# Kernel tuning notes

Hardware: AMD Instinct MI355X
Metric: run time of the kernel (lower is better)

## Reference

```python
import jax, jax.numpy as jnp
import numpy as np

NEG_SLOPE = 0.2  # PyG GATConv default LeakyReLU slope
EPS = 1e-16


def gat_conv(x, src, dst, W, att_src, att_dst, bias, concat):
    """One GATConv layer (PyG semantics, self-loops already in src/dst).
    x: [N, Fin]; src/dst: [E'] int; W: [Fin, H*C]; att_*: [H, C]; bias: [H*C] or [C].
    """
    N = x.shape[0]
    H, C = att_src.shape
    h = (x @ W).reshape(N, H, C)                      # [N, H, C]
    a_s = jnp.einsum('nhc,hc->nh', h, att_src)        # [N, H]
    a_d = jnp.einsum('nhc,hc->nh', h, att_dst)        # [N, H]
    logits = jax.nn.leaky_relu(a_s[src] + a_d[dst], NEG_SLOPE)  # [E', H]
    # segment softmax over incoming edges of each destination node
    m = jax.ops.segment_max(logits, dst, num_segments=N)        # [N, H]
    m = jnp.where(jnp.isfinite(m), m, 0.0)
    e = jnp.exp(logits - m[dst])                                # [E', H]
    denom = jax.ops.segment_sum(e, dst, num_segments=N)         # [N, H]
    alpha = e / (denom[dst] + EPS)                              # [E', H]
    msg = h[src] * alpha[:, :, None]                            # [E', H, C]
    out = jax.ops.segment_sum(msg, dst, num_segments=N)         # [N, H, C]
    out = out.reshape(N, H * C) if concat else out.mean(axis=1)
    return out + bias


def setup_inputs() -> dict:
    key = jax.random.key(0)
    ks = jax.random.split(key, 8)
    N, E, IN, HID, OUT, H1 = 50000, 800000, 128, 64, 32, 2
    x = jax.random.normal(ks[0], (N, IN), dtype=jnp.float32)
    edge_index = jax.random.randint(ks[1], (2, E), 0, N, dtype=jnp.int32)
    # glorot-ish scaled params
    W1 = jax.random.normal(ks[2], (IN, H1 * HID), dtype=jnp.float32) * (1.0 / np.sqrt(IN))
    att_src1 = jax.random.normal(ks[3], (H1, HID), dtype=jnp.float32) * (1.0 / np.sqrt(HID))
    att_dst1 = jax.random.normal(ks[4], (H1, HID), dtype=jnp.float32) * (1.0 / np.sqrt(HID))
    bias1 = jnp.zeros((H1 * HID,), dtype=jnp.float32)
    W2 = jax.random.normal(ks[5], (H1 * HID, OUT), dtype=jnp.float32) * (1.0 / np.sqrt(H1 * HID))
    att_src2 = jax.random.normal(ks[6], (1, OUT), dtype=jnp.float32) * (1.0 / np.sqrt(OUT))
    att_dst2 = jax.random.normal(ks[7], (1, OUT), dtype=jnp.float32) * (1.0 / np.sqrt(OUT))
    bias2 = jnp.zeros((OUT,), dtype=jnp.float32)
    return {"x": x, "edge_index": edge_index, "W1": W1, "att_src1": att_src1,
            "att_dst1": att_dst1, "bias1": bias1, "W2": W2, "att_src2": att_src2,
            "att_dst2": att_dst2, "bias2": bias2}


def reference(x, edge_index, W1, att_src1, att_dst1, bias1, W2, att_src2, att_dst2, bias2):
    N = x.shape[0]
    loops = jnp.arange(N, dtype=edge_index.dtype)
    src = jnp.concatenate([edge_index[0], loops])   # add self loops (PyG default)
    dst = jnp.concatenate([edge_index[1], loops])
    h = gat_conv(x, src, dst, W1, att_src1, att_dst1, bias1, concat=True)
    h = jax.nn.relu(h)
    out = gat_conv(h, src, dst, W2, att_src2, att_dst2, bias2, concat=False)
    return out
```

## Files before the change

### kernel.cpp

```cpp
#include <hip/hip_runtime.h>
#include <math.h>


typedef __bf16 bf16x8 __attribute__((ext_vector_type(8)));
typedef float f32x4 __attribute__((ext_vector_type(4)));

__device__ __forceinline__ float lrelu(float x) { return x > 0.f ? x : 0.2f * x; }

__device__ __forceinline__ unsigned short f2bf(float x) {
  unsigned u = __float_as_uint(x);
  return (unsigned short)((u + 0x7fffu + ((u >> 16) & 1u)) >> 16);
}
__device__ __forceinline__ float2 bf2_unpack(unsigned u) {
  return make_float2(__uint_as_float(u << 16), __uint_as_float(u & 0xffff0000u));
}

constexpr int CAP = 5632;

union SharedK1 {
  struct { int hist[256]; int bbase[256]; } part;
  union { unsigned short bl[32 * 64 * 8]; float accl[64 * 132]; } gem;
};

__launch_bounds__(256)
__global__ void k_csr_gemm1(const int* __restrict__ srcA, const int* __restrict__ dstA,
                            int E, int Nn, int PB, int* __restrict__ gcnt,
                            unsigned* __restrict__ bkt,
                            const float* __restrict__ A, const float* __restrict__ B,
                            unsigned short* __restrict__ Cb,
                            const float* __restrict__ attS, const float* __restrict__ attD,
                            float* __restrict__ asO, float* __restrict__ adO, int M) {
  __shared__ SharedK1 sm;
  const int tid = threadIdx.x;
  if ((int)blockIdx.x < PB) {
    const int NBK = (Nn + 255) >> 8;
    for (int i = tid; i < 256; i += 256) sm.part.hist[i] = 0;
    __syncthreads();
    const int tot = E + Nn;
    const int g0 = blockIdx.x * 4096;
    unsigned pk[16]; int bk[16], rk[16]; int cnt = 0;
#pragma unroll
    for (int j = 0; j < 16; ++j) {
      int g = g0 + j * 256 + tid;
      if (g >= tot) break;
      int s, d;
      if (g < E) { s = srcA[g]; d = dstA[g]; } else { s = g - E; d = s; }
      int b = d >> 8;
      pk[cnt] = (unsigned)s | ((unsigned)(d & 255) << 16);
      bk[cnt] = b;
      rk[cnt] = atomicAdd(&sm.part.hist[b], 1);
      cnt++;
    }
    __syncthreads();
    for (int i = tid; i < 256; i += 256) {
      int h = (i < NBK) ? sm.part.hist[i] : 0;
      sm.part.bbase[i] = h ? atomicAdd(&gcnt[i], h) : 0;
    }
    __syncthreads();
    for (int j = 0; j < cnt; ++j) {
      int pos = sm.part.bbase[bk[j]] + rk[j];
      if (pos < CAP) bkt[(size_t)bk[j] * CAP + pos] = pk[j];
    }
    return;
  }
  const int lane = tid & 63, w = tid >> 6;
  const int row0 = (blockIdx.x - PB) * 64;
  for (int i = tid; i < 128 * 32; i += 256) {
    int k = i >> 5, n4 = (i & 31) << 2;
    float4 v = *(const float4*)(B + k * 128 + n4);
    int c = k >> 5, q = (k >> 3) & 3, j = k & 7;
    float vv[4] = {v.x, v.y, v.z, v.w};
#pragma unroll
    for (int u2 = 0; u2 < 4; ++u2) {
      int n = n4 + u2, t = n >> 4, l = q * 16 + (n & 15);
      sm.gem.bl[((t * 4 + c) * 64 + l) * 8 + j] = f2bf(vv[u2]);
    }
  }
  int mrow = row0 + 16 * w + (lane & 15);
  bool rok = mrow < M;
  const int q = lane >> 4;
  bf16x8 afr[4];
  union { unsigned short s[8]; bf16x8 b; } cv;
#pragma unroll
  for (int c = 0; c < 4; ++c) {
    float4 u0 = make_float4(0.f, 0.f, 0.f, 0.f), u1 = u0;
    if (rok) {
      const float* ap = A + (size_t)mrow * 128 + c * 32 + q * 8;
      u0 = *(const float4*)ap; u1 = *(const float4*)(ap + 4);
    }
    cv.s[0] = f2bf(u0.x); cv.s[1] = f2bf(u0.y); cv.s[2] = f2bf(u0.z); cv.s[3] = f2bf(u0.w);
    cv.s[4] = f2bf(u1.x); cv.s[5] = f2bf(u1.y); cv.s[6] = f2bf(u1.z); cv.s[7] = f2bf(u1.w);
    afr[c] = cv.b;
  }
  __syncthreads();
  f32x4 acc[8];
#pragma unroll
  for (int t = 0; t < 8; ++t) {
    f32x4 a = {0.f, 0.f, 0.f, 0.f};
#pragma unroll
    for (int c = 0; c < 4; ++c) {
      bf16x8 bf = *(((const bf16x8*)sm.gem.bl) + (t * 4 + c) * 64 + lane);
      a = __builtin_amdgcn_mfma_f32_16x16x32_bf16(afr[c], bf, a, 0, 0, 0);
    }
    acc[t] = a;
  }
  __syncthreads();
  {
    int rbase = 16 * w + q * 4, cl = lane & 15;
#pragma unroll
    for (int t = 0; t < 8; ++t)
#pragma unroll
      for (int r = 0; r < 4; ++r)
        sm.gem.accl[(rbase + r) * 132 + 16 * t + cl] = acc[t][r];
  }
  __syncthreads();
  {
    int row = tid >> 2, cg = tid & 3, c0 = cg * 32;
    int grow = row0 + row;
    const float* ar = &sm.gem.accl[row * 132 + c0];
    float ps = 0.f, pd = 0.f;
    unsigned pkv[16];
#pragma unroll
    for (int u2 = 0; u2 < 8; ++u2) {
      float4 v  = *(const float4*)(ar + u2 * 4);
      float4 s4 = *(const float4*)(attS + c0 + u2 * 4);
      float4 d4 = *(const float4*)(attD + c0 + u2 * 4);
      ps += v.x * s4.x + v.y * s4.y + v.z * s4.z + v.w * s4.w;
      pd += v.x * d4.x + v.y * d4.y + v.z * d4.z + v.w * d4.w;
      pkv[u2 * 2]     = (unsigned)f2bf(v.x) | ((unsigned)f2bf(v.y) << 16);
      pkv[u2 * 2 + 1] = (unsigned)f2bf(v.z) | ((unsigned)f2bf(v.w) << 16);
    }
    ps += __shfl_xor(ps, 1); pd += __shfl_xor(pd, 1);
    if (grow < M) {
      if ((tid & 1) == 0) {
        int head = (tid >> 1) & 1;
        asO[(size_t)grow * 2 + head] = ps; adO[(size_t)grow * 2 + head] = pd;
      }
      unsigned* cp = (unsigned*)(Cb + (size_t)grow * 128 + c0);
      *(uint4*)(cp)      = make_uint4(pkv[0], pkv[1], pkv[2], pkv[3]);
      *(uint4*)(cp + 4)  = make_uint4(pkv[4], pkv[5], pkv[6], pkv[7]);
      *(uint4*)(cp + 8)  = make_uint4(pkv[8], pkv[9], pkv[10], pkv[11]);
      *(uint4*)(cp + 12) = make_uint4(pkv[12], pkv[13], pkv[14], pkv[15]);
    }
  }
}

__launch_bounds__(512)
__global__ void k_fine(const unsigned* __restrict__ bkt, const int* __restrict__ gcnt,
                       int Nn, int tot, int* __restrict__ offs, unsigned* __restrict__ csr) {
  __shared__ int fc[256];
  __shared__ int lo[256];
  __shared__ int cur[256];
  __shared__ int baseS;
  const int b = blockIdx.x;
  const int tid = threadIdx.x;
  int m = gcnt[b]; if (m > CAP) m = CAP;
  const unsigned* p = bkt + (size_t)b * CAP;
  if (b == 0 && tid == 0) offs[Nn] = tot;
  for (int i = tid; i < 256; i += 512) fc[i] = 0;
  __syncthreads();
  for (int i = tid; i < m; i += 512) atomicAdd(&fc[p[i] >> 16], 1);
  __syncthreads();
  if (tid < 64) {
    int s = 0;
    for (int c = tid; c < b; c += 64) s += gcnt[c];
#pragma unroll
    for (int o = 32; o; o >>= 1) s += __shfl_xor(s, o);
    if (tid == 0) baseS = s;
    int carry = 0;
    for (int c = 0; c < 256; c += 64) {
      int v = fc[c + tid]; int x = v;
#pragma unroll
      for (int o = 1; o < 64; o <<= 1) { int t = __shfl_up(x, o); if (tid >= o) x += t; }
      lo[c + tid] = carry + x - v;
      carry += __shfl(x, 63);
    }
  }
  __syncthreads();
  const int base = baseS;
  for (int i = tid; i < 256; i += 512) {
    cur[i] = lo[i];
    int n = (b << 8) + i;
    if (n < Nn) offs[n] = base + lo[i];
  }
  __syncthreads();
  for (int i = tid; i < m; i += 512) {
    unsigned e = p[i];
    int pos = atomicAdd(&cur[e >> 16], 1);
    csr[base + pos] = e & 0xffffu;
  }
}

__global__ void k_agg1(const unsigned* __restrict__ h1b, const float* __restrict__ as1,
                       const float* __restrict__ ad1, const int* __restrict__ offs,
                       const unsigned* __restrict__ csr, const float* __restrict__ bias,
                       unsigned* __restrict__ outb, int Nn) {
  int n = blockIdx.x * (blockDim.x >> 6) + (threadIdx.x >> 6);
  if (n >= Nn) return;
  int lane = threadIdx.x & 63;
  int head = lane >> 5;
  int el = lane & 31;
  int pbase = (lane & 32) << 2;
  int beg = offs[n], end = offs[n + 1];
  float2 adn = ((const float2*)ad1)[n];
  float adh = head ? adn.y : adn.x;
  float ax = 0.f, ay = 0.f, den = 0.f;
  int i = beg;
  while (i < end) {
    int m = end - i; if (m > 32) m = 32;
    bool ok = el < m;
    unsigned e = ok ? csr[i + el] : 0u;
    int sv = (int)e;
    float wv = 0.f;
    if (ok) {
      float2 a = ((const float2*)as1)[sv];
      wv = __expf(lrelu((head ? a.y : a.x) + adh));
    }
    int j = 0;
    for (; j + 4 <= m; j += 4) {
#pragma unroll
      for (int u = 0; u < 4; ++u) {
        int s = __builtin_amdgcn_readlane(sv, j + u);
        float ee = __int_as_float(
            __builtin_amdgcn_ds_bpermute(pbase + 4 * (j + u), __float_as_int(wv)));
        float2 v = bf2_unpack(h1b[(size_t)s * 64 + lane]);
        ax += ee * v.x; ay += ee * v.y; den += ee;
      }
    }
    for (; j < m; ++j) {
      int s = __builtin_amdgcn_readlane(sv, j);
      float ee = __int_as_float(
          __builtin_amdgcn_ds_bpermute(pbase + 4 * j, __float_as_int(wv)));
      float2 v = bf2_unpack(h1b[(size_t)s * 64 + lane]);
      ax += ee * v.x; ay += ee * v.y; den += ee;
    }
    i += m;
  }
  float inv = 1.f / (den + 1e-16f);
  const float2 bv = ((const float2*)bias)[lane];
  float o0 = ax * inv + bv.x; o0 = o0 > 0.f ? o0 : 0.f;
  float o1 = ay * inv + bv.y; o1 = o1 > 0.f ? o1 : 0.f;
  outb[(size_t)n * 64 + lane] = (unsigned)f2bf(o0) | ((unsigned)f2bf(o1) << 16);
}

__launch_bounds__(256)
__global__ void k_gemm2(const unsigned* __restrict__ Ab, const float* __restrict__ B,
                        unsigned short* __restrict__ Cb,
                        const float* __restrict__ attS, const float* __restrict__ attD,
                        float* __restrict__ asO, float* __restrict__ adO, int M) {
  __shared__ unsigned short bl[8 * 64 * 8];
  __shared__ float accl[64 * 36];
  const int tid = threadIdx.x;
  const int lane = tid & 63, w = tid >> 6;
  const int row0 = blockIdx.x * 64;
  for (int i = tid; i < 128 * 8; i += 256) {
    int k = i >> 3, n4 = (i & 7) << 2;
    float4 v = *(const float4*)(B + k * 32 + n4);
    int c = k >> 5, q = (k >> 3) & 3, j = k & 7;
    float vv[4] = {v.x, v.y, v.z, v.w};
#pragma unroll
    for (int u2 = 0; u2 < 4; ++u2) {
      int n = n4 + u2, t = n >> 4, l = q * 16 + (n & 15);
      bl[((t * 4 + c) * 64 + l) * 8 + j] = f2bf(vv[u2]);
    }
  }
  int mrow = row0 + 16 * w + (lane & 15);
  bool rok = mrow < M;
  const int q = lane >> 4;
  bf16x8 afr[4];
#pragma unroll
  for (int c = 0; c < 4; ++c) {
    uint4 u = make_uint4(0u, 0u, 0u, 0u);
    if (rok) u = *(const uint4*)(Ab + (size_t)mrow * 64 + c * 16 + q * 4);
    afr[c] = __builtin_bit_cast(bf16x8, u);
  }
  __syncthreads();
  f32x4 acc[2];
#pragma unroll
  for (int t = 0; t < 2; ++t) {
    f32x4 a = {0.f, 0.f, 0.f, 0.f};
#pragma unroll
    for (int c = 0; c < 4; ++c) {
      bf16x8 bf = *(((const bf16x8*)bl) + (t * 4 + c) * 64 + lane);
      a = __builtin_amdgcn_mfma_f32_16x16x32_bf16(afr[c], bf, a, 0, 0, 0);
    }
    acc[t] = a;
  }
  {
    int rbase = 16 * w + q * 4, cl = lane & 15;
#pragma unroll
    for (int t = 0; t < 2; ++t)
#pragma unroll
      for (int r = 0; r < 4; ++r)
        accl[(rbase + r) * 36 + 16 * t + cl] = acc[t][r];
  }
  __syncthreads();
  {
    int row = tid >> 2, cg = tid & 3, c0 = cg * 8;
    int grow = row0 + row;
    const float* ar = &accl[row * 36 + c0];
    float ps = 0.f, pd = 0.f;
    unsigned pk[4];
#pragma unroll
    for (int u2 = 0; u2 < 2; ++u2) {
      float4 v  = *(const float4*)(ar + u2 * 4);
      float4 s4 = *(const float4*)(attS + c0 + u2 * 4);
      float4 d4 = *(const float4*)(attD + c0 + u2 * 4);
      ps += v.x * s4.x + v.y * s4.y + v.z * s4.z + v.w * s4.w;
      pd += v.x * d4.x + v.y * d4.y + v.z * d4.z + v.w * d4.w;
      pk[u2 * 2]     = (unsigned)f2bf(v.x) | ((unsigned)f2bf(v.y) << 16);
      pk[u2 * 2 + 1] = (unsigned)f2bf(v.z) | ((unsigned)f2bf(v.w) << 16);
    }
    ps += __shfl_xor(ps, 1); ps += __shfl_xor(ps, 2);
    pd += __shfl_xor(pd, 1); pd += __shfl_xor(pd, 2);
    if (grow < M) {
      if (cg == 0) { asO[grow] = ps; adO[grow] = pd; }
      *(uint4*)(Cb + (size_t)grow * 32 + c0) = make_uint4(pk[0], pk[1], pk[2], pk[3]);
    }
  }
}

__global__ void k_agg2(const unsigned* __restrict__ h2b, const float* __restrict__ as2,
                       const float* __restrict__ ad2, const int* __restrict__ offs,
                       const unsigned* __restrict__ csr, const float* __restrict__ bias,
                       float* __restrict__ out, int Nn) {
  int n = blockIdx.x * (blockDim.x >> 6) + (threadIdx.x >> 6);
  if (n >= Nn) return;
  int lane = threadIdx.x & 63;
  int g = lane >> 4, cp = lane & 15;
  int beg = offs[n], end = offs[n + 1];
  float adn = ad2[n];
  float ax = 0.f, ay = 0.f, den = 0.f;
  int i = beg;
  while (i < end) {
    int m = end - i; if (m > 64) m = 64;
    int idx = i + lane;
    bool ok = idx < end;
    int sv = ok ? (int)csr[idx] : 0;
    float wv = ok ? __expf(lrelu(as2[sv] + adn)) : 0.f;
    for (int j = 0; j < m; j += 4) {
      int jj = j + g;
      float ee = __shfl(wv, jj);
      int s = __shfl(sv, jj);
      float2 v = bf2_unpack(h2b[(size_t)s * 16 + cp]);
      ax += ee * v.x; ay += ee * v.y; den += ee;
    }
    i += m;
  }
  ax += __shfl_xor(ax, 16); ay += __shfl_xor(ay, 16); den += __shfl_xor(den, 16);
  ax += __shfl_xor(ax, 32); ay += __shfl_xor(ay, 32); den += __shfl_xor(den, 32);
  if (lane < 16) {
    float inv = 1.f / (den + 1e-16f);
    const float2 bv = ((const float2*)bias)[cp];
    ((float2*)out)[(size_t)n * 16 + cp] =
        make_float2(ax * inv + bv.x, ay * inv + bv.y);
  }
}

extern "C" void kernel_launch(void* const* d_in, const int* in_sizes, int n_in,
                              void* d_out, int out_size, void* d_ws, size_t ws_size,
                              hipStream_t stream) {
  const float* x      = (const float*)d_in[0];
  const int*   ei     = (const int*)d_in[1];
  const float* W1     = (const float*)d_in[2];
  const float* att_s1 = (const float*)d_in[3];
  const float* att_d1 = (const float*)d_in[4];
  const float* bias1  = (const float*)d_in[5];
  const float* W2     = (const float*)d_in[6];
  const float* att_s2 = (const float*)d_in[7];
  const float* att_d2 = (const float*)d_in[8];
  const float* bias2  = (const float*)d_in[9];
  float* out = (float*)d_out;

  const int N = in_sizes[0] / 128;
  const int E = in_sizes[1] / 2;
  const int* srcA = ei;
  const int* dstA = ei + E;
  const int tot = E + N;
  const int NBK = (N + 255) >> 8;

  char* w = (char*)d_ws;
  auto alloc = [&](size_t bytes) { char* p = w; w += (bytes + 255) / 256 * 256; return p; };
  unsigned short* h1b = (unsigned short*)alloc((size_t)N * 128 * 2);
  unsigned* h2in_b    = (unsigned*)alloc((size_t)N * 64 * 4);
  unsigned short* h2b = (unsigned short*)alloc((size_t)N * 32 * 2);
  float* as1    = (float*)alloc((size_t)N * 2 * 4);
  float* ad1    = (float*)alloc((size_t)N * 2 * 4);
  float* as2    = (float*)alloc((size_t)N * 4);
  float* ad2    = (float*)alloc((size_t)N * 4);
  int*   gcnt   = (int*)alloc((size_t)NBK * 4);
  unsigned* bkt = (unsigned*)alloc((size_t)NBK * CAP * 4);
  int*   offs   = (int*)alloc((size_t)(N + 1) * 4);
  unsigned* csr = (unsigned*)alloc((size_t)tot * 4);

  hipMemsetAsync(gcnt, 0, (size_t)NBK * 4, stream);

  const int PB = (tot + 4095) / 4096;
  const int GB = (N + 63) / 64;
  k_csr_gemm1<<<PB + GB, 256, 0, stream>>>(srcA, dstA, E, N, PB, gcnt, bkt,
                                           x, W1, h1b, att_s1, att_d1, as1, ad1, N);
  k_fine<<<NBK, 512, 0, stream>>>(bkt, gcnt, N, tot, offs, csr);

  int nb = (N + 3) / 4;
  k_agg1<<<nb, 256, 0, stream>>>((const unsigned*)h1b, as1, ad1, offs, csr, bias1, h2in_b, N);
  k_gemm2<<<GB, 256, 0, stream>>>(h2in_b, W2, h2b, att_s2, att_d2, as2, ad2, N);
  k_agg2<<<nb, 256, 0, stream>>>((const unsigned*)h2b, as2, ad2, offs, csr, bias2, out, N);
}
```

Measured before the change: 195.6 us.

## Fuse CSR fine sort, layer-1 aggregation and second GEMM into one kernel

Buckets shrink from 256 to 64 destination nodes, and one 512-thread block per bucket now does three jobs: it builds the CSR segment in shared memory, aggregates layer 1 for its 64 nodes from that shared edge list, and runs the layer-2 MFMA GEMM from a shared tile. This removes two kernel launches, the global round trip of the layer-1 output, and the re-read of the CSR. The CSR index array also shrinks to 16-bit. In exchange, only about 782 blocks do the aggregation, with each wave handling 8 nodes in sequence, so parallelism drops and load balance may worsen. The per-bucket capacity of 1408 could overflow on skewed graphs.

```diff
diff --git a/kernel.cpp b/kernel.cpp
--- a/kernel.cpp
+++ b/kernel.cpp
@@ -15,10 +15,10 @@
   return make_float2(__uint_as_float(u << 16), __uint_as_float(u & 0xffff0000u));
 }
 
-constexpr int CAP = 5632;
+constexpr int CAP2 = 1408;
 
 union SharedK1 {
-  struct { int hist[256]; int bbase[256]; } part;
+  struct { int hist[1024]; int bbase[1024]; } part;
   union { unsigned short bl[32 * 64 * 8]; float accl[64 * 132]; } gem;
 };
 
@@ -33,8 +33,8 @@
   __shared__ SharedK1 sm;
   const int tid = threadIdx.x;
   if ((int)blockIdx.x < PB) {
-    const int NBK = (Nn + 255) >> 8;
-    for (int i = tid; i < 256; i += 256) sm.part.hist[i] = 0;
+    const int NBK = (Nn + 63) >> 6;
+    for (int i = tid; i < NBK; i += 256) sm.part.hist[i] = 0;
     __syncthreads();
     const int tot = E + Nn;
     const int g0 = blockIdx.x * 4096;
@@ -45,21 +45,21 @@
       if (g >= tot) break;
       int s, d;
       if (g < E) { s = srcA[g]; d = dstA[g]; } else { s = g - E; d = s; }
-      int b = d >> 8;
-      pk[cnt] = (unsigned)s | ((unsigned)(d & 255) << 16);
+      int b = d >> 6;
+      pk[cnt] = (unsigned)s | ((unsigned)(d & 63) << 16);
       bk[cnt] = b;
       rk[cnt] = atomicAdd(&sm.part.hist[b], 1);
       cnt++;
     }
     __syncthreads();
-    for (int i = tid; i < 256; i += 256) {
-      int h = (i < NBK) ? sm.part.hist[i] : 0;
+    for (int i = tid; i < NBK; i += 256) {
+      int h = sm.part.hist[i];
       sm.part.bbase[i] = h ? atomicAdd(&gcnt[i], h) : 0;
     }
     __syncthreads();
     for (int j = 0; j < cnt; ++j) {
       int pos = sm.part.bbase[bk[j]] + rk[j];
-      if (pos < CAP) bkt[(size_t)bk[j] * CAP + pos] = pk[j];
+      if (pos < CAP2) bkt[(size_t)bk[j] * CAP2 + pos] = pk[j];
     }
     return;
   }
@@ -146,18 +146,40 @@
 }
 
 __launch_bounds__(512)
-__global__ void k_fine(const unsigned* __restrict__ bkt, const int* __restrict__ gcnt,
-                       int Nn, int tot, int* __restrict__ offs, unsigned* __restrict__ csr) {
-  __shared__ int fc[256];
-  __shared__ int lo[256];
-  __shared__ int cur[256];
+__global__ void k_fused2(const unsigned* __restrict__ bkt, const int* __restrict__ gcnt,
+                         int Nn, int tot,
+                         const float* __restrict__ as1, const float* __restrict__ ad1,
+                         const float* __restrict__ bias1,
+                         const unsigned* __restrict__ h1b,
+                         const float* __restrict__ W2,
+                         const float* __restrict__ attS, const float* __restrict__ attD,
+                         int* __restrict__ offs, unsigned short* __restrict__ csr16,
+                         unsigned short* __restrict__ h2b,
+                         float* __restrict__ as2, float* __restrict__ ad2) {
+  __shared__ unsigned short bl[8 * 64 * 8];
+  __shared__ unsigned h2t[64 * 68];
+  __shared__ unsigned short srcL[CAP2];
+  __shared__ int fc[64], lo[65], cur[64];
+  __shared__ float accl[64 * 36];
   __shared__ int baseS;
   const int b = blockIdx.x;
   const int tid = threadIdx.x;
-  int m = gcnt[b]; if (m > CAP) m = CAP;
-  const unsigned* p = bkt + (size_t)b * CAP;
-  if (b == 0 && tid == 0) offs[Nn] = tot;
-  for (int i = tid; i < 256; i += 512) fc[i] = 0;
+  int m = gcnt[b]; if (m > CAP2) m = CAP2;
+  const unsigned* p = bkt + (size_t)b * CAP2;
+
+  for (int i = tid; i < 128 * 8; i += 512) {
+    int k = i >> 3, n4 = (i & 7) << 2;
+    float4 v = *(const float4*)(W2 + k * 32 + n4);
+    int c = k >> 5, q = (k >> 3) & 3, j = k & 7;
+    float vv[4] = {v.x, v.y, v.z, v.w};
+#pragma unroll
+    for (int u2 = 0; u2 < 4; ++u2) {
+      int n = n4 + u2, t = n >> 4, l = q * 16 + (n & 15);
+      bl[((t * 4 + c) * 64 + l) * 8 + j] = f2bf(vv[u2]);
+    }
+  }
+  if (tid < 64) fc[tid] = 0;
+  if (b == 0 && tid == 64) offs[Nn] = tot;
   __syncthreads();
   for (int i = tid; i < m; i += 512) atomicAdd(&fc[p[i] >> 16], 1);
   __syncthreads();
@@ -167,140 +189,104 @@
 #pragma unroll
     for (int o = 32; o; o >>= 1) s += __shfl_xor(s, o);
     if (tid == 0) baseS = s;
-    int carry = 0;
-    for (int c = 0; c < 256; c += 64) {
-      int v = fc[c + tid]; int x = v;
-#pragma unroll
-      for (int o = 1; o < 64; o <<= 1) { int t = __shfl_up(x, o); if (tid >= o) x += t; }
-      lo[c + tid] = carry + x - v;
-      carry += __shfl(x, 63);
-    }
-  }
-  __syncthreads();
-  const int base = baseS;
-  for (int i = tid; i < 256; i += 512) {
-    cur[i] = lo[i];
-    int n = (b << 8) + i;
-    if (n < Nn) offs[n] = base + lo[i];
+    int v = fc[tid], x = v;
+#pragma unroll
+    for (int o = 1; o < 64; o <<= 1) { int t = __shfl_up(x, o); if (tid >= o) x += t; }
+    lo[tid] = x - v;
+    cur[tid] = x - v;
+    if (tid == 63) lo[64] = x;
   }
   __syncthreads();
   for (int i = tid; i < m; i += 512) {
     unsigned e = p[i];
     int pos = atomicAdd(&cur[e >> 16], 1);
-    csr[base + pos] = e & 0xffffu;
-  }
-}
-
-__global__ void k_agg1(const unsigned* __restrict__ h1b, const float* __restrict__ as1,
-                       const float* __restrict__ ad1, const int* __restrict__ offs,
-                       const unsigned* __restrict__ csr, const float* __restrict__ bias,
-                       unsigned* __restrict__ outb, int Nn) {
-  int n = blockIdx.x * (blockDim.x >> 6) + (threadIdx.x >> 6);
-  if (n >= Nn) return;
-  int lane = threadIdx.x & 63;
-  int head = lane >> 5;
-  int el = lane & 31;
-  int pbase = (lane & 32) << 2;
-  int beg = offs[n], end = offs[n + 1];
-  float2 adn = ((const float2*)ad1)[n];
-  float adh = head ? adn.y : adn.x;
-  float ax = 0.f, ay = 0.f, den = 0.f;
-  int i = beg;
-  while (i < end) {
-    int m = end - i; if (m > 32) m = 32;
-    bool ok = el < m;
-    unsigned e = ok ? csr[i + el] : 0u;
-    int sv = (int)e;
-    float wv = 0.f;
-    if (ok) {
-      float2 a = ((const float2*)as1)[sv];
-      wv = __expf(lrelu((head ? a.y : a.x) + adh));
-    }
-    int j = 0;
-    for (; j + 4 <= m; j += 4) {
-#pragma unroll
-      for (int u = 0; u < 4; ++u) {
-        int s = __builtin_amdgcn_readlane(sv, j + u);
+    srcL[pos] = (unsigned short)(e & 0xffffu);
+  }
+  __syncthreads();
+  const int base = baseS;
+  for (int i = tid; i < m; i += 512) csr16[base + i] = srcL[i];
+  if (tid < 64) {
+    int n = (b << 6) + tid;
+    if (n < Nn) offs[n] = base + lo[tid];
+  }
+
+  const int w = tid >> 6, lane = tid & 63;
+  const int head = lane >> 5, el = lane & 31;
+  const int pbase = (lane & 32) << 2;
+  for (int j8 = 0; j8 < 8; ++j8) {
+    int j = w * 8 + j8;
+    int n = (b << 6) + j;
+    if (n >= Nn) break;
+    int beg = lo[j], end = lo[j + 1];
+    float2 adn = ((const float2*)ad1)[n];
+    float adh = head ? adn.y : adn.x;
+    float ax = 0.f, ay = 0.f, den = 0.f;
+    int i = beg;
+    while (i < end) {
+      int mm = end - i; if (mm > 32) mm = 32;
+      bool ok = el < mm;
+      int sv = ok ? (int)srcL[i + el] : 0;
+      float wv = 0.f;
+      if (ok) {
+        float2 a = ((const float2*)as1)[sv];
+        wv = __expf(lrelu((head ? a.y : a.x) + adh));
+      }
+      int j2 = 0;
+      for (; j2 + 4 <= mm; j2 += 4) {
+#pragma unroll
+        for (int u = 0; u < 4; ++u) {
+          int s = __builtin_amdgcn_readlane(sv, j2 + u);
+          float ee = __int_as_float(
+              __builtin_amdgcn_ds_bpermute(pbase + 4 * (j2 + u), __float_as_int(wv)));
+          float2 v = bf2_unpack(h1b[(size_t)s * 64 + lane]);
+          ax += ee * v.x; ay += ee * v.y; den += ee;
+        }
+      }
+      for (; j2 < mm; ++j2) {
+        int s = __builtin_amdgcn_readlane(sv, j2);
         float ee = __int_as_float(
-            __builtin_amdgcn_ds_bpermute(pbase + 4 * (j + u), __float_as_int(wv)));
+            __builtin_amdgcn_ds_bpermute(pbase + 4 * j2, __float_as_int(wv)));
         float2 v = bf2_unpack(h1b[(size_t)s * 64 + lane]);
         ax += ee * v.x; ay += ee * v.y; den += ee;
       }
-    }
-    for (; j < m; ++j) {
-      int s = __builtin_amdgcn_readlane(sv, j);
-      float ee = __int_as_float(
-          __builtin_amdgcn_ds_bpermute(pbase + 4 * j, __float_as_int(wv)));
-      float2 v = bf2_unpack(h1b[(size_t)s * 64 + lane]);
-      ax += ee * v.x; ay += ee * v.y; den += ee;
-    }
-    i += m;
-  }
-  float inv = 1.f / (den + 1e-16f);
-  const float2 bv = ((const float2*)bias)[lane];
-  float o0 = ax * inv + bv.x; o0 = o0 > 0.f ? o0 : 0.f;
-  float o1 = ay * inv + bv.y; o1 = o1 > 0.f ? o1 : 0.f;
-  outb[(size_t)n * 64 + lane] = (unsigned)f2bf(o0) | ((unsigned)f2bf(o1) << 16);
-}
-
-__launch_bounds__(256)
-__global__ void k_gemm2(const unsigned* __restrict__ Ab, const float* __restrict__ B,
-                        unsigned short* __restrict__ Cb,
-                        const float* __restrict__ attS, const float* __restrict__ attD,
-                        float* __restrict__ asO, float* __restrict__ adO, int M) {
-  __shared__ unsigned short bl[8 * 64 * 8];
-  __shared__ float accl[64 * 36];
-  const int tid = threadIdx.x;
-  const int lane = tid & 63, w = tid >> 6;
-  const int row0 = blockIdx.x * 64;
-  for (int i = tid; i < 128 * 8; i += 256) {
-    int k = i >> 3, n4 = (i & 7) << 2;
-    float4 v = *(const float4*)(B + k * 32 + n4);
-    int c = k >> 5, q = (k >> 3) & 3, j = k & 7;
-    float vv[4] = {v.x, v.y, v.z, v.w};
-#pragma unroll
-    for (int u2 = 0; u2 < 4; ++u2) {
-      int n = n4 + u2, t = n >> 4, l = q * 16 + (n & 15);
-      bl[((t * 4 + c) * 64 + l) * 8 + j] = f2bf(vv[u2]);
-    }
-  }
-  int mrow = row0 + 16 * w + (lane & 15);
-  bool rok = mrow < M;
-  const int q = lane >> 4;
-  bf16x8 afr[4];
-#pragma unroll
-  for (int c = 0; c < 4; ++c) {
-    uint4 u = make_uint4(0u, 0u, 0u, 0u);
-    if (rok) u = *(const uint4*)(Ab + (size_t)mrow * 64 + c * 16 + q * 4);
-    afr[c] = __builtin_bit_cast(bf16x8, u);
-  }
-  __syncthreads();
-  f32x4 acc[2];
-#pragma unroll
-  for (int t = 0; t < 2; ++t) {
+      i += mm;
+    }
+    float inv = 1.f / (den + 1e-16f);
+    const float2 bv = ((const float2*)bias1)[lane];
+    float o0 = ax * inv + bv.x; o0 = o0 > 0.f ? o0 : 0.f;
+    float o1 = ay * inv + bv.y; o1 = o1 > 0.f ? o1 : 0.f;
+    h2t[j * 68 + lane] = (unsigned)f2bf(o0) | ((unsigned)f2bf(o1) << 16);
+  }
+  __syncthreads();
+
+  {
+    int rt = w & 3, ct = w >> 2;
+    int mloc = rt * 16 + (lane & 15);
+    int q = lane >> 4;
+    bf16x8 afr[4];
+#pragma unroll
+    for (int c = 0; c < 4; ++c) {
+      uint4 u = *(const uint4*)&h2t[mloc * 68 + c * 16 + q * 4];
+      afr[c] = __builtin_bit_cast(bf16x8, u);
+    }
     f32x4 a = {0.f, 0.f, 0.f, 0.f};
 #pragma unroll
     for (int c = 0; c < 4; ++c) {
-      bf16x8 bf = *(((const bf16x8*)bl) + (t * 4 + c) * 64 + lane);
+      bf16x8 bf = *(((const bf16x8*)bl) + (ct * 4 + c) * 64 + lane);
       a = __builtin_amdgcn_mfma_f32_16x16x32_bf16(afr[c], bf, a, 0, 0, 0);
     }
-    acc[t] = a;
-  }
-  {
-    int rbase = 16 * w + q * 4, cl = lane & 15;
-#pragma unroll
-    for (int t = 0; t < 2; ++t)
-#pragma unroll
-      for (int r = 0; r < 4; ++r)
-        accl[(rbase + r) * 36 + 16 * t + cl] = acc[t][r];
-  }
-  __syncthreads();
-  {
+    int rbase = rt * 16 + q * 4, cl = lane & 15;
+#pragma unroll
+    for (int r = 0; r < 4; ++r)
+      accl[(rbase + r) * 36 + ct * 16 + cl] = a[r];
+  }
+  __syncthreads();
+  if (tid < 256) {
     int row = tid >> 2, cg = tid & 3, c0 = cg * 8;
-    int grow = row0 + row;
+    int grow = (b << 6) + row;
     const float* ar = &accl[row * 36 + c0];
     float ps = 0.f, pd = 0.f;
-    unsigned pk[4];
+    unsigned pkv[4];
 #pragma unroll
     for (int u2 = 0; u2 < 2; ++u2) {
       float4 v  = *(const float4*)(ar + u2 * 4);
@@ -308,22 +294,22 @@
       float4 d4 = *(const float4*)(attD + c0 + u2 * 4);
       ps += v.x * s4.x + v.y * s4.y + v.z * s4.z + v.w * s4.w;
       pd += v.x * d4.x + v.y * d4.y + v.z * d4.z + v.w * d4.w;
-      pk[u2 * 2]     = (unsigned)f2bf(v.x) | ((unsigned)f2bf(v.y) << 16);
-      pk[u2 * 2 + 1] = (unsigned)f2bf(v.z) | ((unsigned)f2bf(v.w) << 16);
+      pkv[u2 * 2]     = (unsigned)f2bf(v.x) | ((unsigned)f2bf(v.y) << 16);
+      pkv[u2 * 2 + 1] = (unsigned)f2bf(v.z) | ((unsigned)f2bf(v.w) << 16);
     }
     ps += __shfl_xor(ps, 1); ps += __shfl_xor(ps, 2);
     pd += __shfl_xor(pd, 1); pd += __shfl_xor(pd, 2);
-    if (grow < M) {
-      if (cg == 0) { asO[grow] = ps; adO[grow] = pd; }
-      *(uint4*)(Cb + (size_t)grow * 32 + c0) = make_uint4(pk[0], pk[1], pk[2], pk[3]);
+    if (grow < Nn) {
+      if (cg == 0) { as2[grow] = ps; ad2[grow] = pd; }
+      *(uint4*)(h2b + (size_t)grow * 32 + c0) = make_uint4(pkv[0], pkv[1], pkv[2], pkv[3]);
     }
   }
 }
 
 __global__ void k_agg2(const unsigned* __restrict__ h2b, const float* __restrict__ as2,
                        const float* __restrict__ ad2, const int* __restrict__ offs,
-                       const unsigned* __restrict__ csr, const float* __restrict__ bias,
-                       float* __restrict__ out, int Nn) {
+                       const unsigned short* __restrict__ csr16,
+                       const float* __restrict__ bias, float* __restrict__ out, int Nn) {
   int n = blockIdx.x * (blockDim.x >> 6) + (threadIdx.x >> 6);
   if (n >= Nn) return;
   int lane = threadIdx.x & 63;
@@ -336,7 +322,7 @@
     int m = end - i; if (m > 64) m = 64;
     int idx = i + lane;
     bool ok = idx < end;
-    int sv = ok ? (int)csr[idx] : 0;
+    int sv = ok ? (int)csr16[idx] : 0;
     float wv = ok ? __expf(lrelu(as2[sv] + adn)) : 0.f;
     for (int j = 0; j < m; j += 4) {
       int jj = j + g;
@@ -377,21 +363,20 @@
   const int* srcA = ei;
   const int* dstA = ei + E;
   const int tot = E + N;
-  const int NBK = (N + 255) >> 8;
+  const int NBK = (N + 63) >> 6;
 
   char* w = (char*)d_ws;
   auto alloc = [&](size_t bytes) { char* p = w; w += (bytes + 255) / 256 * 256; return p; };
   unsigned short* h1b = (unsigned short*)alloc((size_t)N * 128 * 2);
-  unsigned* h2in_b    = (unsigned*)alloc((size_t)N * 64 * 4);
   unsigned short* h2b = (unsigned short*)alloc((size_t)N * 32 * 2);
   float* as1    = (float*)alloc((size_t)N * 2 * 4);
   float* ad1    = (float*)alloc((size_t)N * 2 * 4);
   float* as2    = (float*)alloc((size_t)N * 4);
   float* ad2    = (float*)alloc((size_t)N * 4);
   int*   gcnt   = (int*)alloc((size_t)NBK * 4);
-  unsigned* bkt = (unsigned*)alloc((size_t)NBK * CAP * 4);
+  unsigned* bkt = (unsigned*)alloc((size_t)NBK * CAP2 * 4);
   int*   offs   = (int*)alloc((size_t)(N + 1) * 4);
-  unsigned* csr = (unsigned*)alloc((size_t)tot * 4);
+  unsigned short* csr16 = (unsigned short*)alloc((size_t)tot * 2);
 
   hipMemsetAsync(gcnt, 0, (size_t)NBK * 4, stream);
 
@@ -399,10 +384,9 @@
   const int GB = (N + 63) / 64;
   k_csr_gemm1<<<PB + GB, 256, 0, stream>>>(srcA, dstA, E, N, PB, gcnt, bkt,
                                            x, W1, h1b, att_s1, att_d1, as1, ad1, N);
-  k_fine<<<NBK, 512, 0, stream>>>(bkt, gcnt, N, tot, offs, csr);
-
+  k_fused2<<<NBK, 512, 0, stream>>>(bkt, gcnt, N, tot, as1, ad1, bias1,
+                                    (const unsigned*)h1b, W2, att_s2, att_d2,
+                                    offs, csr16, h2b, as2, ad2);
   int nb = (N + 3) / 4;
-  k_agg1<<<nb, 256, 0, stream>>>((const unsigned*)h1b, as1, ad1, offs, csr, bias1, h2in_b, N);
-  k_gemm2<<<GB, 256, 0, stream>>>(h2in_b, W2, h2b, att_s2, att_d2, as2, ad2, N);
-  k_agg2<<<nb, 256, 0, stream>>>((const unsigned*)h2b, as2, ad2, offs, csr, bias2, out, N);
-}
+  k_agg2<<<nb, 256, 0, stream>>>((const unsigned*)h2b, as2, ad2, offs, csr16, bias2, out, N);
+}
```

After: 181.9 us. -7.0%, faster.
